# Optimization experiments

Hardware: AMD Instinct MI355X
Metric: run time of the kernel (lower is better)

## Reference

```python
import jax, jax.numpy as jnp
import numpy as np

L = 16; F = 2; T = 1 << 19; BASE = 16.0; FINEST = 2048.0; CDIM = 16; N = 262144
_PRIMES = np.array([1, 2654435761, 805459861], dtype=np.uint32)
_OFFS = np.array([[i, j, k] for i in (0, 1) for j in (0, 1) for k in (0, 1)], dtype=np.uint32)
_RES = np.floor(BASE * np.exp(np.arange(L) * (np.log(FINEST) - np.log(BASE)) / (L - 1))).astype(np.float32)


def _hash_encode(pn, table):
    # pn: [N,3] normalized to [0,1]; table: [L,T,F]
    offs = jnp.asarray(_OFFS)
    offs_mask = jnp.asarray(_OFFS.astype(bool))
    primes = jnp.asarray(_PRIMES)

    def level(tab, res):
        scaled = pn * res
        pos = jnp.floor(scaled)
        frac = scaled - pos
        corners = pos.astype(jnp.uint32)[:, None, :] + offs[None]  # [N,8,3]
        idx = (corners[..., 0] * primes[0]) ^ (corners[..., 1] * primes[1]) ^ (corners[..., 2] * primes[2])
        idx = (idx & jnp.uint32(T - 1)).astype(jnp.int32)
        feats = tab[idx]  # [N,8,F]
        w = jnp.prod(jnp.where(offs_mask[None], frac[:, None, :], 1.0 - frac[:, None, :]), axis=-1)  # [N,8]
        return jnp.einsum('nkf,nk->nf', feats, w)

    out = jax.vmap(level)(table, jnp.asarray(_RES))  # [L,N,F]
    return jnp.transpose(out, (1, 0, 2)).reshape(pn.shape[0], L * F)


def _lin(x, w, b):
    return x @ w.T + b


def _forward(p, bound, t_sdf, t_color, t_sem,
             f_w0, f_b0, f_w1, f_b1, f_w2, f_b2, f_w3, f_b3,
             osdf_w, osdf_b, orgb_w0, orgb_b0, orgb_w1, orgb_b1,
             s_w0, s_b0, s_w1, s_b1, s_w2, s_b2, s_wo, s_bo):
    pn = (p - bound[:, 0]) / (bound[:, 1] - bound[:, 0])
    feat = _hash_encode(pn, t_sdf)    # [N,32]
    c_feat = _hash_encode(pn, t_color)
    s_feat = _hash_encode(pn, t_sem)
    h = feat
    for w, b in ((f_w0, f_b0), (f_w1, f_b1), (f_w2, f_b2), (f_w3, f_b3)):
        h = jax.nn.relu(_lin(h, w, b))
    sdf_out = _lin(h, osdf_w, osdf_b)        # [N,17]
    sdf = jnp.tanh(sdf_out[:, 0])            # [N]
    sdf_feat = sdf_out[:, 1:]                # [N,16]
    rgb_in = jnp.concatenate([sdf_feat, c_feat, s_feat], axis=-1)  # [N,80]
    rgb = jax.nn.sigmoid(_lin(jax.nn.relu(_lin(rgb_in, orgb_w0, orgb_b0)), orgb_w1, orgb_b1))  # [N,3]
    hs = s_feat
    for w, b in ((s_w0, s_b0), (s_w1, s_b1), (s_w2, s_b2)):
        hs = jax.nn.relu(_lin(hs, w, b))
    semantic = _lin(hs, s_wo, s_bo)          # [N,25]
    raw = jnp.concatenate([rgb, sdf[:, None], semantic], axis=-1)  # [N,29]
    plane_feat = jnp.concatenate([c_feat[:, CDIM:], feat[:, CDIM:], s_feat[:, CDIM:]], axis=-1)  # [N,48]
    return raw, plane_feat


def setup_inputs() -> dict:
    key = jax.random.key(0)
    ks = jax.random.split(key, 32)

    def w(k, o, i):
        return (jax.random.normal(k, (o, i), jnp.float32) / np.sqrt(i)).astype(jnp.float32)

    return {
        'p': jax.random.uniform(ks[0], (N, 3), jnp.float32),
        'bound': jnp.array([[0.0, 1.0], [0.0, 1.0], [0.0, 1.0]], jnp.float32),
        't_sdf': jax.random.uniform(ks[1], (L, T, F), jnp.float32, -1e-2, 1e-2),
        't_color': jax.random.uniform(ks[2], (L, T, F), jnp.float32, -1e-2, 1e-2),
        't_sem': jax.random.uniform(ks[3], (L, T, F), jnp.float32, -1e-2, 1e-2),
        'f_w0': w(ks[4], 16, 32), 'f_b0': jnp.zeros(16, jnp.float32),
        'f_w1': w(ks[5], 16, 16), 'f_b1': jnp.zeros(16, jnp.float32),
        'f_w2': w(ks[6], 16, 16), 'f_b2': jnp.zeros(16, jnp.float32),
        'f_w3': w(ks[7], 16, 16), 'f_b3': jnp.zeros(16, jnp.float32),
        'osdf_w': w(ks[8], 17, 16), 'osdf_b': jnp.zeros(17, jnp.float32),
        'orgb_w0': w(ks[9], 16, 80), 'orgb_b0': jnp.zeros(16, jnp.float32),
        'orgb_w1': w(ks[10], 3, 16), 'orgb_b1': jnp.zeros(3, jnp.float32),
        's_w0': w(ks[11], 256, 32), 's_b0': jnp.zeros(256, jnp.float32),
        's_w1': w(ks[12], 256, 256), 's_b1': jnp.zeros(256, jnp.float32),
        's_w2': w(ks[13], 256, 256), 's_b2': jnp.zeros(256, jnp.float32),
        's_wo': w(ks[14], 25, 256), 's_bo': jnp.zeros(25, jnp.float32),
    }


def reference(p, bound, t_sdf, t_color, t_sem,
              f_w0, f_b0, f_w1, f_b1, f_w2, f_b2, f_w3, f_b3,
              osdf_w, osdf_b, orgb_w0, orgb_b0, orgb_w1, orgb_b1,
              s_w0, s_b0, s_w1, s_b1, s_w2, s_b2, s_wo, s_bo):
    return _forward(p, bound, t_sdf, t_color, t_sem,
                    f_w0, f_b0, f_w1, f_b1, f_w2, f_b2, f_w3, f_b3,
                    osdf_w, osdf_b, orgb_w0, orgb_b0, orgb_w1, orgb_b1,
                    s_w0, s_b0, s_w1, s_b1, s_w2, s_b2, s_wo, s_bo)
```

## Files before the change

kernel.cpp:

```cpp
#include <hip/hip_runtime.h>
#include <math.h>

#define NPTS 262144
#define TTAB 524288
#define TMASK (TTAB - 1)
#define PR1 2654435761u
#define PR2 805459861u

#define MQ_SLOTS 512
#define MHASH_BLOCKS (8 * MQ_SLOTS)
#define FQ_SLOTS 1536
#define FHASH_BLOCKS (8 * FQ_SLOTS)

typedef __attribute__((ext_vector_type(4))) float f32x4;
typedef __attribute__((ext_vector_type(8))) short bf16x8;
typedef __attribute__((ext_vector_type(3))) unsigned int uintx3;

struct ResArr { float r[16]; };

__device__ __forceinline__ float bf2f(unsigned int u) {
  union { unsigned int i; float f; } v; v.i = u << 16; return v.f;
}
__device__ __forceinline__ unsigned short f2bf(float f) {
  union { float f; unsigned int i; } v; v.f = f;
  unsigned int r = v.i + 0x7FFFu + ((v.i >> 16) & 1u);
  return (unsigned short)(r >> 16);
}
__device__ __forceinline__ unsigned int pack2(float a, float b) {
  return (unsigned int)f2bf(a) | ((unsigned int)f2bf(b) << 16);
}
__device__ __forceinline__ unsigned int cvtpk(float lo, float hi) {
  unsigned int r;
  asm("v_cvt_pk_bf16_f32 %0, %1, %2" : "=v"(r) : "v"(lo), "v"(hi));
  return r;
}

union U8 { uint4 u; bf16x8 v; };

__global__ __launch_bounds__(256) void cvt_tab(
    const float* __restrict__ t0, const float* __restrict__ t1,
    const float* __restrict__ t2, unsigned int* __restrict__ mt)
{
  size_t i = (size_t)blockIdx.x * 256 + threadIdx.x;
  float2 a = ((const float2*)t0)[i];
  float2 b = ((const float2*)t1)[i];
  float2 c = ((const float2*)t2)[i];
  mt[i * 3 + 0] = pack2(a.x, a.y);
  mt[i * 3 + 1] = pack2(b.x, b.y);
  mt[i * 3 + 2] = pack2(c.x, c.y);
}

__global__ __launch_bounds__(256) void hash_merged(
    const float* __restrict__ p, const float* __restrict__ bound,
    const unsigned int* __restrict__ mt,
    unsigned int* __restrict__ featws, unsigned int* __restrict__ ctr,
    ResArr res)
{
  __shared__ int s_slot;
  if (threadIdx.x == 0) {
    unsigned int xcc;
    asm volatile("s_getreg_b32 %0, hwreg(HW_REG_XCC_ID)" : "=s"(xcc));
    xcc &= 7u;
    int slot = -1;
    for (int k = 0; k < 8; ++k) {
      unsigned int q = (xcc + (unsigned int)k) & 7u;
      unsigned int s = atomicAdd(ctr + q, 1u);
      if (s < MQ_SLOTS) { slot = (int)(q * MQ_SLOTS + s); break; }
    }
    s_slot = slot;
  }
  __syncthreads();
  int slot = s_slot;
  if (slot < 0) return;

  unsigned int q = (unsigned int)slot / MQ_SLOTS;
  unsigned int s = (unsigned int)slot - q * MQ_SLOTS;
  unsigned int level = (s >> 8) * 8u + q;
  unsigned int chunk = s & 255u;

  float r = res.r[0];
#pragma unroll
  for (int l = 1; l < 16; ++l) r = (level == (unsigned int)l) ? res.r[l] : r;

  float b0 = bound[0], b1 = bound[1], b2 = bound[2], b3 = bound[3],
        b4 = bound[4], b5 = bound[5];
  float i0v = 1.f / (b1 - b0), i1v = 1.f / (b3 - b2), i2v = 1.f / (b5 - b4);
  const unsigned int* mtl = mt + (size_t)level * TTAB * 3u;
  unsigned int f0 = (0u * 16u + level) * (unsigned int)NPTS;
  unsigned int f1 = (1u * 16u + level) * (unsigned int)NPTS;
  unsigned int f2b = (2u * 16u + level) * (unsigned int)NPTS;
  unsigned int nbase = chunk * 1024u + threadIdx.x;

#pragma unroll
  for (int half = 0; half < 2; ++half) {
    unsigned int CX[2], CY[2], CZ[2];
    float DX[2], DY[2], DZ[2];
#pragma unroll
    for (int pt = 0; pt < 2; ++pt) {
      unsigned int n = nbase + (unsigned int)(half * 512 + pt * 256);
      float px = p[n * 3 + 0], py = p[n * 3 + 1], pz = p[n * 3 + 2];
      float sx = (px - b0) * i0v * r;
      float sy = (py - b2) * i1v * r;
      float sz = (pz - b4) * i2v * r;
      float fx = floorf(sx), fy = floorf(sy), fz = floorf(sz);
      DX[pt] = sx - fx; DY[pt] = sy - fy; DZ[pt] = sz - fz;
      CX[pt] = (unsigned int)fx;
      CY[pt] = (unsigned int)fy * PR1;
      CZ[pt] = (unsigned int)fz * PR2;
    }
    __builtin_amdgcn_sched_barrier(0);

    uintx3 V[2][8];
#pragma unroll
    for (int pt = 0; pt < 2; ++pt) {
      unsigned int x0 = CX[pt], x1 = CX[pt] + 1u;
      unsigned int y0 = CY[pt], y1 = y0 + PR1;
      unsigned int z0 = CZ[pt], z1 = z0 + PR2;
      unsigned int id[8];
      id[0] = (x0 ^ y0 ^ z0) & TMASK;
      id[1] = (x0 ^ y0 ^ z1) & TMASK;
      id[2] = (x0 ^ y1 ^ z0) & TMASK;
      id[3] = (x0 ^ y1 ^ z1) & TMASK;
      id[4] = (x1 ^ y0 ^ z0) & TMASK;
      id[5] = (x1 ^ y0 ^ z1) & TMASK;
      id[6] = (x1 ^ y1 ^ z0) & TMASK;
      id[7] = (x1 ^ y1 ^ z1) & TMASK;
#pragma unroll
      for (int c = 0; c < 8; ++c)
        V[pt][c] = *(const uintx3*)(mtl + (size_t)id[c] * 3u);
    }
    __builtin_amdgcn_sched_barrier(0);

#pragma unroll
    for (int pt = 0; pt < 2; ++pt) {
      float dx = DX[pt], dy = DY[pt], dz = DZ[pt];
      float wx[2] = { 1.f - dx, dx }, wy[2] = { 1.f - dy, dy }, wz[2] = { 1.f - dz, dz };
      float a00 = 0.f, a01 = 0.f, a10 = 0.f, a11 = 0.f, a20 = 0.f, a21 = 0.f;
#pragma unroll
      for (int c = 0; c < 8; ++c) {
        float w = wx[c >> 2] * wy[(c >> 1) & 1] * wz[c & 1];
        unsigned int u0 = V[pt][c].x, u1 = V[pt][c].y, u2 = V[pt][c].z;
        a00 += bf2f(u0 << 16) * w;  a01 += bf2f(u0 & 0xFFFF0000u) * w;
        a10 += bf2f(u1 << 16) * w;  a11 += bf2f(u1 & 0xFFFF0000u) * w;
        a20 += bf2f(u2 << 16) * w;  a21 += bf2f(u2 & 0xFFFF0000u) * w;
      }
      unsigned int n = nbase + (unsigned int)(half * 512 + pt * 256);
      featws[f0 + n] = pack2(a00, a01);
      featws[f1 + n] = pack2(a10, a11);
      featws[f2b + n] = pack2(a20, a21);
    }
  }
}

__global__ __launch_bounds__(256) void hash_f32(
    const float* __restrict__ p, const float* __restrict__ bound,
    const float* __restrict__ t0, const float* __restrict__ t1,
    const float* __restrict__ t2,
    unsigned int* __restrict__ featws, unsigned int* __restrict__ ctr,
    ResArr res)
{
  __shared__ int s_pad[10240];
  if (threadIdx.x == 0) {
    unsigned int xcc;
    asm volatile("s_getreg_b32 %0, hwreg(HW_REG_XCC_ID)" : "=s"(xcc));
    xcc &= 7u;
    int slot = -1;
    for (int k = 0; k < 8; ++k) {
      unsigned int q = (xcc + (unsigned int)k) & 7u;
      unsigned int s = atomicAdd(ctr + q, 1u);
      if (s < FQ_SLOTS) { slot = (int)(q * FQ_SLOTS + s); break; }
    }
    s_pad[0] = slot;
  }
  __syncthreads();
  int slot = s_pad[0];
  if (slot < 0) return;

  unsigned int q = (unsigned int)slot / FQ_SLOTS;
  unsigned int s = (unsigned int)slot - q * FQ_SLOTS;
  unsigned int i = (s >> 8) * 8u + q;
  unsigned int level = i / 3u;
  unsigned int table = i - level * 3u;
  unsigned int chunk = s & 255u;

  float r = res.r[0];
#pragma unroll
  for (int l = 1; l < 16; ++l) r = (level == (unsigned int)l) ? res.r[l] : r;

  float b0 = bound[0], b1 = bound[1], b2 = bound[2], b3 = bound[3],
        b4 = bound[4], b5 = bound[5];
  const float* tf = ((table == 0u) ? t0 : (table == 1u) ? t1 : t2) +
                    (size_t)level * (TTAB * 2);
  unsigned int fbase = (table * 16u + level) * (unsigned int)NPTS;
  unsigned int nbase = chunk * 1024u + threadIdx.x;

#pragma unroll
  for (int it = 0; it < 4; ++it) {
    unsigned int n = nbase + (unsigned int)it * 256u;
    float px = p[n * 3 + 0], py = p[n * 3 + 1], pz = p[n * 3 + 2];
    float x = (px - b0) / (b1 - b0);
    float y = (py - b2) / (b3 - b2);
    float z = (pz - b4) / (b5 - b4);
    float sx = x * r, sy = y * r, sz = z * r;
    float fx = floorf(sx), fy = floorf(sy), fz = floorf(sz);
    float dx = sx - fx, dy = sy - fy, dz = sz - fz;
    unsigned int cx = (unsigned int)fx, cy = (unsigned int)fy, cz = (unsigned int)fz;
    unsigned int hx[2] = { cx, cx + 1u };
    unsigned int hy[2] = { cy * PR1, (cy + 1u) * PR1 };
    unsigned int hz[2] = { cz * PR2, (cz + 1u) * PR2 };
    float wx[2] = { 1.f - dx, dx }, wy[2] = { 1.f - dy, dy }, wz[2] = { 1.f - dz, dz };
    float a0 = 0.f, a1 = 0.f;
#pragma unroll
    for (int ii = 0; ii < 2; ++ii)
#pragma unroll
      for (int jj = 0; jj < 2; ++jj)
#pragma unroll
        for (int kk = 0; kk < 2; ++kk) {
          unsigned int idx = (hx[ii] ^ hy[jj] ^ hz[kk]) & TMASK;
          float2 f2 = *(const float2*)(tf + (size_t)idx * 2);
          float w = wx[ii] * wy[jj] * wz[kk];
          a0 += f2.x * w;
          a1 += f2.y * w;
        }
    featws[fbase + n] = pack2(a0, a1);
  }
}

__global__ __launch_bounds__(256) void mlp_small_kernel(
    const unsigned int* __restrict__ fws,
    const float* __restrict__ fw0, const float* __restrict__ fb0,
    const float* __restrict__ fw1, const float* __restrict__ fb1,
    const float* __restrict__ fw2, const float* __restrict__ fb2,
    const float* __restrict__ fw3, const float* __restrict__ fb3,
    const float* __restrict__ ow, const float* __restrict__ ob,
    const float* __restrict__ rw0, const float* __restrict__ rb0,
    const float* __restrict__ rw1, const float* __restrict__ rb1,
    float* __restrict__ out)
{
  unsigned int n = blockIdx.x * 256 + threadIdx.x;
  float ft[32], cf[32], sf[32];
#pragma unroll
  for (int l = 0; l < 16; ++l) {
    unsigned int u = fws[(0u * 16 + l) * (unsigned int)NPTS + n];
    ft[2 * l] = bf2f(u << 16); ft[2 * l + 1] = bf2f(u & 0xFFFF0000u);
    u = fws[(1u * 16 + l) * (unsigned int)NPTS + n];
    cf[2 * l] = bf2f(u << 16); cf[2 * l + 1] = bf2f(u & 0xFFFF0000u);
    u = fws[(2u * 16 + l) * (unsigned int)NPTS + n];
    sf[2 * l] = bf2f(u << 16); sf[2 * l + 1] = bf2f(u & 0xFFFF0000u);
  }

  {
    float* pf = out + (size_t)NPTS * 29 + (size_t)n * 48;
#pragma unroll
    for (int i2 = 0; i2 < 16; i2 += 4)
      *(float4*)(pf + i2) = make_float4(cf[16 + i2], cf[17 + i2], cf[18 + i2], cf[19 + i2]);
#pragma unroll
    for (int i2 = 0; i2 < 16; i2 += 4)
      *(float4*)(pf + 16 + i2) = make_float4(ft[16 + i2], ft[17 + i2], ft[18 + i2], ft[19 + i2]);
#pragma unroll
    for (int i2 = 0; i2 < 16; i2 += 4)
      *(float4*)(pf + 32 + i2) = make_float4(sf[16 + i2], sf[17 + i2], sf[18 + i2], sf[19 + i2]);
  }

  float h[16], g[16];
  for (int o = 0; o < 16; ++o) {
    float a = fb0[o];
    for (int i2 = 0; i2 < 32; ++i2) a += ft[i2] * fw0[o * 32 + i2];
    h[o] = fmaxf(a, 0.f);
  }
  for (int o = 0; o < 16; ++o) {
    float a = fb1[o];
    for (int i2 = 0; i2 < 16; ++i2) a += h[i2] * fw1[o * 16 + i2];
    g[o] = fmaxf(a, 0.f);
  }
  for (int o = 0; o < 16; ++o) {
    float a = fb2[o];
    for (int i2 = 0; i2 < 16; ++i2) a += g[i2] * fw2[o * 16 + i2];
    h[o] = fmaxf(a, 0.f);
  }
  for (int o = 0; o < 16; ++o) {
    float a = fb3[o];
    for (int i2 = 0; i2 < 16; ++i2) a += h[i2] * fw3[o * 16 + i2];
    g[o] = fmaxf(a, 0.f);
  }
  float so[17];
  for (int o = 0; o < 17; ++o) {
    float a = ob[o];
    for (int i2 = 0; i2 < 16; ++i2) a += g[i2] * ow[o * 16 + i2];
    so[o] = a;
  }
  float sdf = tanhf(so[0]);
  float rin[80];
#pragma unroll
  for (int i2 = 0; i2 < 16; ++i2) rin[i2] = so[i2 + 1];
#pragma unroll
  for (int i2 = 0; i2 < 32; ++i2) rin[16 + i2] = cf[i2];
#pragma unroll
  for (int i2 = 0; i2 < 32; ++i2) rin[48 + i2] = sf[i2];
  float hr[16];
  for (int o = 0; o < 16; ++o) {
    float a = rb0[o];
    for (int i2 = 0; i2 < 80; ++i2) a += rin[i2] * rw0[o * 80 + i2];
    hr[o] = fmaxf(a, 0.f);
  }
  float* po = out + (size_t)n * 29;
  for (int o = 0; o < 3; ++o) {
    float a = rb1[o];
    for (int i2 = 0; i2 < 16; ++i2) a += hr[i2] * rw1[o * 16 + i2];
    po[o] = 1.f / (1.f + expf(-a));
  }
  po[3] = sdf;
}

__global__ __launch_bounds__(256) void cvt_kernel(
    const float* __restrict__ sw0, const float* __restrict__ sw1,
    const float* __restrict__ sw2, const float* __restrict__ swo,
    unsigned short* __restrict__ w0, unsigned short* __restrict__ w1,
    unsigned short* __restrict__ w2, unsigned short* __restrict__ wo,
    unsigned int* __restrict__ ctr)
{
  int t = blockIdx.x * 256 + threadIdx.x;
  if (t < 8) ctr[t] = 0u;
  if (t < 8192) w0[t] = f2bf(sw0[t]);
  w1[t] = f2bf(sw1[t]);
  w2[t] = f2bf(sw2[t]);
  if (t < 8192) wo[t] = (t < 6400) ? f2bf(swo[t]) : (unsigned short)0;
}

#define LAYER256(Wp, Bp)                                                                   \
  {                                                                                        \
    _Pragma("unroll") for (int r = 0; r < 8; ++r)                                          \
      _Pragma("unroll") for (int c = 0; c < 2; ++c)                                        \
        acc[r][c] = (f32x4){0.f, 0.f, 0.f, 0.f};                                           \
    _Pragma("unroll") for (int c = 0; c < 2; ++c) {                                        \
      bc[c] = *(const bf16x8*)(Wp + (size_t)(cw + 2 * l16 + c) * 256 + quad * 8);          \
      bn[c] = *(const bf16x8*)(Wp + (size_t)(cw + 2 * l16 + c) * 256 + 32 + quad * 8);     \
    }                                                                                      \
    _Pragma("unroll") for (int ks = 0; ks < 8; ++ks) {                                     \
      int k0 = ks * 32;                                                                    \
      if (ks < 6) {                                                                        \
        _Pragma("unroll") for (int c = 0; c < 2; ++c)                                      \
          bn2[c] = *(const bf16x8*)(Wp + (size_t)(cw + 2 * l16 + c) * 256 + k0 + 64 + quad * 8); \
      }                                                                                    \
      __builtin_amdgcn_s_setprio(1);                                                       \
      _Pragma("unroll") for (int r = 0; r < 8; ++r) {                                      \
        bf16x8 av = *(const bf16x8*)(H + (r * 16 + l16) * 264 + k0 + quad * 8);            \
        acc[r][0] = __builtin_amdgcn_mfma_f32_16x16x32_bf16(av, bc[0], acc[r][0], 0, 0, 0);\
        acc[r][1] = __builtin_amdgcn_mfma_f32_16x16x32_bf16(av, bc[1], acc[r][1], 0, 0, 0);\
      }                                                                                    \
      __builtin_amdgcn_s_setprio(0);                                                       \
      _Pragma("unroll") for (int c = 0; c < 2; ++c) { bc[c] = bn[c]; bn[c] = bn2[c]; }     \
    }                                                                                      \
    __syncthreads();                                         \
    {                                                                                      \
      float2 bias2 = *(const float2*)(Bp + cw + 2 * l16);                                  \
      _Pragma("unroll") for (int r = 0; r < 8; ++r)                                        \
        _Pragma("unroll") for (int g2 = 0; g2 < 4; ++g2) {                                 \
          float lo = fmaxf(acc[r][0][g2] + bias2.x, 0.f);                                  \
          float hi = fmaxf(acc[r][1][g2] + bias2.y, 0.f);                                  \
          int row = r * 16 + quad * 4 + g2;                                                \
          *(unsigned int*)(H + row * 264 + cw + 2 * l16) = cvtpk(lo, hi);                  \
        }                                                                                  \
    }                                                                                      \
    __syncthreads();                                                   \
  }

__global__ __launch_bounds__(512, 4) void sem_kernel(
    const unsigned int* __restrict__ fws,
    const unsigned short* __restrict__ w0, const unsigned short* __restrict__ w1,
    const unsigned short* __restrict__ w2, const unsigned short* __restrict__ wo,
    const float* __restrict__ b0, const float* __restrict__ b1,
    const float* __restrict__ b2, const float* __restrict__ bo,
    float* __restrict__ out)
{
  __shared__ alignas(16) unsigned short H[128 * 264];

  int tid = threadIdx.x;
  int n0 = blockIdx.x * 128;
  int lane = tid & 63, wv = tid >> 6;
  int l16 = lane & 15, quad = lane >> 4;
  int cw = wv * 32;

  f32x4 acc[8][2];
  bf16x8 bc[2], bn[2], bn2[2];

#pragma unroll
  for (int r = 0; r < 8; ++r)
#pragma unroll
    for (int c = 0; c < 2; ++c) acc[r][c] = (f32x4){0.f, 0.f, 0.f, 0.f};
#pragma unroll
  for (int c = 0; c < 2; ++c)
    bc[c] = *(const bf16x8*)(w0 + (size_t)(cw + 2 * l16 + c) * 32 + quad * 8);
#pragma unroll
  for (int r = 0; r < 8; ++r) {
    unsigned int base = (32u + (unsigned int)quad * 4u) * (unsigned int)NPTS +
                        (unsigned int)(n0 + r * 16 + l16);
    U8 u;
    u.u.x = fws[base];
    u.u.y = fws[base + (unsigned int)NPTS];
    u.u.z = fws[base + 2u * (unsigned int)NPTS];
    u.u.w = fws[base + 3u * (unsigned int)NPTS];
    acc[r][0] = __builtin_amdgcn_mfma_f32_16x16x32_bf16(u.v, bc[0], acc[r][0], 0, 0, 0);
    acc[r][1] = __builtin_amdgcn_mfma_f32_16x16x32_bf16(u.v, bc[1], acc[r][1], 0, 0, 0);
  }
  {
    float2 bias2 = *(const float2*)(b0 + cw + 2 * l16);
#pragma unroll
    for (int r = 0; r < 8; ++r)
#pragma unroll
      for (int g2 = 0; g2 < 4; ++g2) {
        float lo = fmaxf(acc[r][0][g2] + bias2.x, 0.f);
        float hi = fmaxf(acc[r][1][g2] + bias2.y, 0.f);
        int row = r * 16 + quad * 4 + g2;
        *(unsigned int*)(H + row * 264 + cw + 2 * l16) = cvtpk(lo, hi);
      }
  }
  __syncthreads();

  LAYER256(w1, b1)
  LAYER256(w2, b2)

  {
    f32x4 acc2[2];
    acc2[0] = (f32x4){0.f, 0.f, 0.f, 0.f};
    acc2[1] = (f32x4){0.f, 0.f, 0.f, 0.f};
#pragma unroll
    for (int ks = 0; ks < 8; ++ks) {
      int k0 = ks * 32;
      bf16x8 af = *(const bf16x8*)(H + (wv * 16 + l16) * 264 + k0 + quad * 8);
#pragma unroll
      for (int c = 0; c < 2; ++c) {
        bf16x8 bfr = *(const bf16x8*)(wo + (size_t)(c * 16 + l16) * 256 + k0 + quad * 8);
        acc2[c] = __builtin_amdgcn_mfma_f32_16x16x32_bf16(af, bfr, acc2[c], 0, 0, 0);
      }
    }
#pragma unroll
    for (int c = 0; c < 2; ++c) {
      int col = c * 16 + l16;
      if (col < 25) {
        float bias = bo[col];
#pragma unroll
        for (int g2 = 0; g2 < 4; ++g2) {
          int row = wv * 16 + quad * 4 + g2;
          out[(size_t)(n0 + row) * 29 + 4 + col] = acc2[c][g2] + bias;
        }
      }
    }
  }
}

extern "C" void kernel_launch(void* const* d_in, const int* in_sizes, int n_in,
                              void* d_out, int out_size, void* d_ws, size_t ws_size,
                              hipStream_t stream) {
  const float* p      = (const float*)d_in[0];
  const float* bound  = (const float*)d_in[1];
  const float* t_sdf  = (const float*)d_in[2];
  const float* t_color= (const float*)d_in[3];
  const float* t_sem  = (const float*)d_in[4];
  const float* f_w0   = (const float*)d_in[5];
  const float* f_b0   = (const float*)d_in[6];
  const float* f_w1   = (const float*)d_in[7];
  const float* f_b1   = (const float*)d_in[8];
  const float* f_w2   = (const float*)d_in[9];
  const float* f_b2   = (const float*)d_in[10];
  const float* f_w3   = (const float*)d_in[11];
  const float* f_b3   = (const float*)d_in[12];
  const float* osdf_w = (const float*)d_in[13];
  const float* osdf_b = (const float*)d_in[14];
  const float* orgb_w0= (const float*)d_in[15];
  const float* orgb_b0= (const float*)d_in[16];
  const float* orgb_w1= (const float*)d_in[17];
  const float* orgb_b1= (const float*)d_in[18];
  const float* s_w0   = (const float*)d_in[19];
  const float* s_b0   = (const float*)d_in[20];
  const float* s_w1   = (const float*)d_in[21];
  const float* s_b1   = (const float*)d_in[22];
  const float* s_w2   = (const float*)d_in[23];
  const float* s_b2   = (const float*)d_in[24];
  const float* s_wo   = (const float*)d_in[25];
  const float* s_bo   = (const float*)d_in[26];

  unsigned int* featws = (unsigned int*)d_ws;
  unsigned short* w0b = (unsigned short*)(featws + 48u * NPTS);
  unsigned short* w1b = w0b + 8192;
  unsigned short* w2b = w1b + 65536;
  unsigned short* wob = w2b + 65536;
  unsigned int* ctr = (unsigned int*)(wob + 8192);
  unsigned int* mt = ctr + 8;
  size_t need_bt = ((char*)mt - (char*)d_ws) + (size_t)16 * TTAB * 12;
  bool use_bt = ws_size >= need_bt;

  ResArr res;
  double kk = (log(2048.0) - log(16.0)) / 15.0;
  for (int l = 0; l < 16; ++l) res.r[l] = (float)floor(16.0 * exp((double)l * kk));

  float* out = (float*)d_out;

  hipLaunchKernelGGL(cvt_kernel, dim3(256), dim3(256), 0, stream,
                     s_w0, s_w1, s_w2, s_wo, w0b, w1b, w2b, wob, ctr);
  if (use_bt) {
    hipLaunchKernelGGL(cvt_tab, dim3(32768), dim3(256), 0, stream,
                       t_sdf, t_color, t_sem, mt);
    hipLaunchKernelGGL(hash_merged, dim3(MHASH_BLOCKS), dim3(256), 0, stream,
                       p, bound, mt, featws, ctr, res);
  } else {
    hipLaunchKernelGGL(hash_f32, dim3(FHASH_BLOCKS), dim3(256), 0, stream,
                       p, bound, t_sdf, t_color, t_sem, featws, ctr, res);
  }
  hipLaunchKernelGGL(mlp_small_kernel, dim3(1024), dim3(256), 0, stream,
                     featws, f_w0, f_b0, f_w1, f_b1, f_w2, f_b2, f_w3, f_b3,
                     osdf_w, osdf_b, orgb_w0, orgb_b0, orgb_w1, orgb_b1, out);
  hipLaunchKernelGGL(sem_kernel, dim3(NPTS / 128), dim3(512), 0, stream,
                     featws, w0b, w1b, w2b, wob, s_b0, s_b1, s_b2, s_bo, out);
}
```

Measured before the change: 512.2 us.

## Switch semantic MLP layers to 32x32x16 MFMA with double-buffered LDS A fragments

Replaces the 16x16x32 bf16 MFMA tiling in the semantic MLP (first layer and the two 256-wide layers) with 32x32x16 MFMA tiles. Each wave now computes four 32x32 output tiles, and A fragments from LDS are prefetched one k-step ahead into a double buffer. The epilogue writes single bf16 values using software rounding instead of packed cvt stores. The aim is fewer MFMA instructions and fewer LDS reads of A per FLOP, at the cost of more scalar 16-bit LDS stores in the epilogue and possibly higher register pressure.

```diff
diff --git a/kernel.cpp b/kernel.cpp
--- a/kernel.cpp
+++ b/kernel.cpp
@@ -13,6 +13,7 @@
 #define FHASH_BLOCKS (8 * FQ_SLOTS)
 
 typedef __attribute__((ext_vector_type(4))) float f32x4;
+typedef __attribute__((ext_vector_type(16))) float f32x16;
 typedef __attribute__((ext_vector_type(8))) short bf16x8;
 typedef __attribute__((ext_vector_type(3))) unsigned int uintx3;
 
@@ -28,11 +29,6 @@
 }
 __device__ __forceinline__ unsigned int pack2(float a, float b) {
   return (unsigned int)f2bf(a) | ((unsigned int)f2bf(b) << 16);
-}
-__device__ __forceinline__ unsigned int cvtpk(float lo, float hi) {
-  unsigned int r;
-  asm("v_cvt_pk_bf16_f32 %0, %1, %2" : "=v"(r) : "v"(lo), "v"(hi));
-  return r;
 }
 
 union U8 { uint4 u; bf16x8 v; };
@@ -329,37 +325,34 @@
 
 #define LAYER256(Wp, Bp)                                                                   \
   {                                                                                        \
-    _Pragma("unroll") for (int r = 0; r < 8; ++r)                                          \
-      _Pragma("unroll") for (int c = 0; c < 2; ++c)                                        \
-        acc[r][c] = (f32x4){0.f, 0.f, 0.f, 0.f};                                           \
-    _Pragma("unroll") for (int c = 0; c < 2; ++c) {                                        \
-      bc[c] = *(const bf16x8*)(Wp + (size_t)(cw + 2 * l16 + c) * 256 + quad * 8);          \
-      bn[c] = *(const bf16x8*)(Wp + (size_t)(cw + 2 * l16 + c) * 256 + 32 + quad * 8);     \
-    }                                                                                      \
-    _Pragma("unroll") for (int ks = 0; ks < 8; ++ks) {                                     \
-      int k0 = ks * 32;                                                                    \
-      if (ks < 6) {                                                                        \
-        _Pragma("unroll") for (int c = 0; c < 2; ++c)                                      \
-          bn2[c] = *(const bf16x8*)(Wp + (size_t)(cw + 2 * l16 + c) * 256 + k0 + 64 + quad * 8); \
+    _Pragma("unroll") for (int rt = 0; rt < 4; ++rt)                                       \
+      _Pragma("unroll") for (int g = 0; g < 16; ++g) acc[rt][g] = 0.f;                     \
+    bc = *(const bf16x8*)(Wp + (size_t)(cw + l32) * 256 + hi * 8);                         \
+    bn = *(const bf16x8*)(Wp + (size_t)(cw + l32) * 256 + 16 + hi * 8);                    \
+    _Pragma("unroll") for (int rt = 0; rt < 4; ++rt)                                       \
+      a2[0][rt] = *(const bf16x8*)(H + (rt * 32 + l32) * 264 + hi * 8);                    \
+    _Pragma("unroll") for (int ks = 0; ks < 16; ++ks) {                                    \
+      int k0 = ks * 16;                                                                    \
+      if (ks < 14)                                                                         \
+        bn2 = *(const bf16x8*)(Wp + (size_t)(cw + l32) * 256 + k0 + 32 + hi * 8);          \
+      if (ks < 15) {                                                                       \
+        _Pragma("unroll") for (int rt = 0; rt < 4; ++rt)                                   \
+          a2[(ks + 1) & 1][rt] =                                                           \
+              *(const bf16x8*)(H + (rt * 32 + l32) * 264 + k0 + 16 + hi * 8);              \
       }                                                                                    \
       __builtin_amdgcn_s_setprio(1);                                                       \
-      _Pragma("unroll") for (int r = 0; r < 8; ++r) {                                      \
-        bf16x8 av = *(const bf16x8*)(H + (r * 16 + l16) * 264 + k0 + quad * 8);            \
-        acc[r][0] = __builtin_amdgcn_mfma_f32_16x16x32_bf16(av, bc[0], acc[r][0], 0, 0, 0);\
-        acc[r][1] = __builtin_amdgcn_mfma_f32_16x16x32_bf16(av, bc[1], acc[r][1], 0, 0, 0);\
-      }                                                                                    \
+      _Pragma("unroll") for (int rt = 0; rt < 4; ++rt)                                     \
+        acc[rt] = __builtin_amdgcn_mfma_f32_32x32x16_bf16(a2[ks & 1][rt], bc, acc[rt], 0, 0, 0); \
       __builtin_amdgcn_s_setprio(0);                                                       \
-      _Pragma("unroll") for (int c = 0; c < 2; ++c) { bc[c] = bn[c]; bn[c] = bn2[c]; }     \
+      bc = bn; bn = bn2;                                                                   \
     }                                                                                      \
     __syncthreads();                                         \
     {                                                                                      \
-      float2 bias2 = *(const float2*)(Bp + cw + 2 * l16);                                  \
-      _Pragma("unroll") for (int r = 0; r < 8; ++r)                                        \
-        _Pragma("unroll") for (int g2 = 0; g2 < 4; ++g2) {                                 \
-          float lo = fmaxf(acc[r][0][g2] + bias2.x, 0.f);                                  \
-          float hi = fmaxf(acc[r][1][g2] + bias2.y, 0.f);                                  \
-          int row = r * 16 + quad * 4 + g2;                                                \
-          *(unsigned int*)(H + row * 264 + cw + 2 * l16) = cvtpk(lo, hi);                  \
+      float bias = Bp[cw + l32];                                                           \
+      _Pragma("unroll") for (int rt = 0; rt < 4; ++rt)                                     \
+        _Pragma("unroll") for (int g = 0; g < 16; ++g) {                                   \
+          int row = rt * 32 + (g & 3) + 8 * (g >> 2) + 4 * hi;                             \
+          H[row * 264 + cw + l32] = f2bf(fmaxf(acc[rt][g] + bias, 0.f));                   \
         }                                                                                  \
     }                                                                                      \
     __syncthreads();                                                   \
@@ -378,41 +371,41 @@
   int tid = threadIdx.x;
   int n0 = blockIdx.x * 128;
   int lane = tid & 63, wv = tid >> 6;
+  int l32 = lane & 31, hi = lane >> 5;
   int l16 = lane & 15, quad = lane >> 4;
   int cw = wv * 32;
 
-  f32x4 acc[8][2];
-  bf16x8 bc[2], bn[2], bn2[2];
-
-#pragma unroll
-  for (int r = 0; r < 8; ++r)
-#pragma unroll
-    for (int c = 0; c < 2; ++c) acc[r][c] = (f32x4){0.f, 0.f, 0.f, 0.f};
-#pragma unroll
-  for (int c = 0; c < 2; ++c)
-    bc[c] = *(const bf16x8*)(w0 + (size_t)(cw + 2 * l16 + c) * 32 + quad * 8);
-#pragma unroll
-  for (int r = 0; r < 8; ++r) {
-    unsigned int base = (32u + (unsigned int)quad * 4u) * (unsigned int)NPTS +
-                        (unsigned int)(n0 + r * 16 + l16);
-    U8 u;
-    u.u.x = fws[base];
-    u.u.y = fws[base + (unsigned int)NPTS];
-    u.u.z = fws[base + 2u * (unsigned int)NPTS];
-    u.u.w = fws[base + 3u * (unsigned int)NPTS];
-    acc[r][0] = __builtin_amdgcn_mfma_f32_16x16x32_bf16(u.v, bc[0], acc[r][0], 0, 0, 0);
-    acc[r][1] = __builtin_amdgcn_mfma_f32_16x16x32_bf16(u.v, bc[1], acc[r][1], 0, 0, 0);
+  f32x16 acc[4];
+  bf16x8 a2[2][4], bc, bn, bn2;
+
+#pragma unroll
+  for (int rt = 0; rt < 4; ++rt)
+#pragma unroll
+    for (int g = 0; g < 16; ++g) acc[rt][g] = 0.f;
+#pragma unroll
+  for (int ks = 0; ks < 2; ++ks) {
+    int k0 = ks * 16;
+    bc = *(const bf16x8*)(w0 + (size_t)(cw + l32) * 32 + k0 + hi * 8);
+#pragma unroll
+    for (int rt = 0; rt < 4; ++rt) {
+      unsigned int base = (32u + (unsigned int)(k0 / 2) + (unsigned int)hi * 4u) * (unsigned int)NPTS +
+                          (unsigned int)(n0 + rt * 32 + l32);
+      U8 u;
+      u.u.x = fws[base];
+      u.u.y = fws[base + (unsigned int)NPTS];
+      u.u.z = fws[base + 2u * (unsigned int)NPTS];
+      u.u.w = fws[base + 3u * (unsigned int)NPTS];
+      acc[rt] = __builtin_amdgcn_mfma_f32_32x32x16_bf16(u.v, bc, acc[rt], 0, 0, 0);
+    }
   }
   {
-    float2 bias2 = *(const float2*)(b0 + cw + 2 * l16);
-#pragma unroll
-    for (int r = 0; r < 8; ++r)
-#pragma unroll
-      for (int g2 = 0; g2 < 4; ++g2) {
-        float lo = fmaxf(acc[r][0][g2] + bias2.x, 0.f);
-        float hi = fmaxf(acc[r][1][g2] + bias2.y, 0.f);
-        int row = r * 16 + quad * 4 + g2;
-        *(unsigned int*)(H + row * 264 + cw + 2 * l16) = cvtpk(lo, hi);
+    float bias = b0[cw + l32];
+#pragma unroll
+    for (int rt = 0; rt < 4; ++rt)
+#pragma unroll
+      for (int g = 0; g < 16; ++g) {
+        int row = rt * 32 + (g & 3) + 8 * (g >> 2) + 4 * hi;
+        H[row * 264 + cw + l32] = f2bf(fmaxf(acc[rt][g] + bias, 0.f));
       }
   }
   __syncthreads();
```

Result: no change. 514.0 us (+0.3%).
